# Kernel tuning notes

Measured on AMD Instinct MI355X. Metric: run time of the kernel, lower is better.

## Reference

```python
import jax, jax.numpy as jnp
import numpy as np

N_POINTS = 2097152
N_LEVELS = 16
F_PER_LEVEL = 2
LOG2_T = 19
T = 1 << LOG2_T            # 524288 entries per level
BASE_RES = 16
GROWTH = 1.5
PRIME_Y = np.uint32(2654435761)  # tcnn 2D spatial-hash prime (dim 0 prime is 1)


def _level_encode(x, tab, level):
    """Bilinear hash-grid lookup for one level. x: [N,2] in [0,1], tab: [T,F]."""
    scale = BASE_RES * GROWTH ** level - 1.0          # python float, static
    res = int(np.ceil(scale)) + 1                     # grid resolution (static)
    dense = res * res <= T                            # tcnn: dense if grid fits

    pos = x * jnp.asarray(scale, x.dtype) + 0.5       # [N,2]
    pg = jnp.floor(pos)
    frac = pos - pg                                   # [N,2] interpolation weights
    pg = pg.astype(jnp.uint32)

    out = jnp.zeros((x.shape[0], F_PER_LEVEL), x.dtype)
    for dx in (0, 1):
        for dy in (0, 1):
            cx = pg[:, 0] + np.uint32(dx)
            cy = pg[:, 1] + np.uint32(dy)
            if dense:
                idx = (cx + cy * np.uint32(res)) % np.uint32(T)
            else:
                idx = (cx ^ (cy * PRIME_Y)) % np.uint32(T)
            wx = frac[:, 0] if dx else 1.0 - frac[:, 0]
            wy = frac[:, 1] if dy else 1.0 - frac[:, 1]
            out = out + tab[idx.astype(jnp.int32)] * (wx * wy)[:, None]
    return out  # [N, F]


def setup_inputs() -> dict:
    key = jax.random.key(0)
    k1, k2 = jax.random.split(key)
    x = jax.random.uniform(k1, (N_POINTS, 2), dtype=jnp.float32)
    # tcnn initializes hash-grid params uniform in [-1e-4, 1e-4]
    table = jax.random.uniform(k2, (N_LEVELS, T, F_PER_LEVEL), dtype=jnp.float32,
                               minval=-1e-4, maxval=1e-4)
    return {"x": x, "table": table}


def reference(x, table):
    # multiresolution hash encoding: per-level bilinear gather, concat features
    outs = [_level_encode(x, table[l], l) for l in range(N_LEVELS)]
    return jnp.concatenate(outs, axis=-1)  # [N, N_LEVELS * F_PER_LEVEL] = [N, 32]
```

## Files before the change

### kernel.cpp

```cpp
#include <hip/hip_runtime.h>
#include <stdint.h>


constexpr int      kNPoints = 2097152;
constexpr uint32_t kT       = 524288u;
constexpr uint32_t kTMask   = kT - 1u;
constexpr uint32_t kPrimeY  = 2654435761u;

__device__ __host__ inline void level_consts(int l, float& sc, uint32_t& re, int& dense) {
    const float ksc[16] = {
        15.0f, 23.0f, 35.0f, 53.0f, 80.0f, 120.5f, 181.25f, 272.375f,
        409.0625f, 614.09375f, 921.640625f, 1382.9609375f,
        2074.94140625f, 3112.912109375f, 4669.8681640625f, 7005.30224609375f};
    const uint32_t kre[16] = {16u, 24u, 36u, 54u, 81u, 122u, 183u, 274u,
                              411u, 616u, 923u, 1384u, 2076u, 3114u, 4671u, 7007u};
    sc = ksc[l]; re = kre[l]; dense = (l < 10) ? 1 : 0;
}

__device__ __forceinline__ float2 encode_one(float2 xy, float scale, uint32_t res,
                                             int dense, const float2* __restrict__ tab) {
    const float px  = __fadd_rn(__fmul_rn(xy.x, scale), 0.5f);
    const float py  = __fadd_rn(__fmul_rn(xy.y, scale), 0.5f);
    const float fpx = floorf(px);
    const float fpy = floorf(py);
    const float fx  = px - fpx;
    const float fy  = py - fpy;
    const uint32_t gx = (uint32_t)fpx;
    const uint32_t gy = (uint32_t)fpy;

    float ax = 0.0f, ay = 0.0f;
#pragma unroll
    for (int dx = 0; dx < 2; ++dx) {
        const uint32_t cx = gx + (uint32_t)dx;
        const float    wx = dx ? fx : (1.0f - fx);
#pragma unroll
        for (int dy = 0; dy < 2; ++dy) {
            const uint32_t cy = gy + (uint32_t)dy;
            const float    wy = dy ? fy : (1.0f - fy);
            const uint32_t idx_d = (cx + cy * res) & kTMask;
            const uint32_t idx_h = (cx ^ (cy * kPrimeY)) & kTMask;
            const uint32_t idx   = dense ? idx_d : idx_h;
            const float2   v     = tab[idx];
            const float    w     = wx * wy;
            ax = fmaf(v.x, w, ax);
            ay = fmaf(v.y, w, ay);
        }
    }
    return make_float2(ax, ay);
}

__global__ __launch_bounds__(256) void level_kernel(
    const float* __restrict__ x,
    const float2* __restrict__ tab,
    float2* __restrict__ wsl,
    float scale, uint32_t res, int dense)
{
    const uint32_t n  = blockIdx.x * 256 + threadIdx.x;
    const float2   xy = reinterpret_cast<const float2*>(x)[n];
    const float2   r  = encode_one(xy, scale, res, dense, tab);
    union { float2 f2; unsigned long long u64; } p; p.f2 = r;
    __builtin_nontemporal_store(p.u64, reinterpret_cast<unsigned long long*>(wsl) + n);
}

template <int SPLIT>
__global__ __launch_bounds__(256) void merge_kernel(
    const float* __restrict__ x,
    const float* __restrict__ table,
    const float2* __restrict__ ws,
    float* __restrict__ out)
{
    __shared__ float s[256 * 36];
    const uint32_t tid = threadIdx.x;
    const uint32_t n   = blockIdx.x * 256 + tid;
    const float2   xy  = reinterpret_cast<const float2*>(x)[n];

#pragma unroll
    for (int l = 0; l < SPLIT; ++l) {
        float sc; uint32_t re; int de;
        level_consts(l, sc, re, de);
        const float2* tab = reinterpret_cast<const float2*>(table) + ((size_t)l << 19);
        const float2 r = encode_one(xy, sc, re, de, tab);
        s[tid * 36 + 2 * l]     = r.x;
        s[tid * 36 + 2 * l + 1] = r.y;
    }
#pragma unroll
    for (int j = 0; j < 16 - SPLIT; ++j) {
        const float2 v = ws[(size_t)j * kNPoints + n];
        s[tid * 36 + 2 * (SPLIT + j)]     = v.x;
        s[tid * 36 + 2 * (SPLIT + j) + 1] = v.y;
    }
    __syncthreads();

    float4* outb = reinterpret_cast<float4*>(out + (size_t)blockIdx.x * 8192);
#pragma unroll
    for (int k = 0; k < 8; ++k) {
        const uint32_t q   = tid + k * 256;
        const uint32_t row = q >> 3;
        const uint32_t c   = (q & 7u) * 4u;
        const float* sp = &s[row * 36 + c];
        outb[q] = make_float4(sp[0], sp[1], sp[2], sp[3]);
    }
}

__global__ __launch_bounds__(256) void hashgrid_fwd_fallback(
    const float* __restrict__ x,
    const float* __restrict__ table,
    float* __restrict__ out)
{
    const uint32_t tid = blockIdx.x * blockDim.x + threadIdx.x;
    const uint32_t l   = tid & 15u;
    const uint32_t n   = tid >> 4;
    float sc; uint32_t re; int de;
    level_consts((int)l, sc, re, de);
    const float2 xy = reinterpret_cast<const float2*>(x)[n];
    const float2* tab = reinterpret_cast<const float2*>(table) + ((size_t)l << 19);
    const float2 r = encode_one(xy, sc, re, de, tab);
    reinterpret_cast<float2*>(out)[tid] = r;
}

extern "C" void kernel_launch(void* const* d_in, const int* in_sizes, int n_in,
                              void* d_out, int out_size, void* d_ws, size_t ws_size,
                              hipStream_t stream) {
    const float* x     = (const float*)d_in[0];
    const float* table = (const float*)d_in[1];
    float*       out   = (float*)d_out;
    const int nblk = kNPoints / 256;

    const size_t need8 = (size_t)8 * kNPoints * sizeof(float2);
    const size_t need6 = (size_t)6 * kNPoints * sizeof(float2);

    if (ws_size >= need8) {
        float2* ws = (float2*)d_ws;
        for (int l = 8; l < 16; ++l) {
            float sc; uint32_t re; int de;
            level_consts(l, sc, re, de);
            level_kernel<<<nblk, 256, 0, stream>>>(
                x, reinterpret_cast<const float2*>(table) + ((size_t)l << 19),
                ws + (size_t)(l - 8) * kNPoints, sc, re, de);
        }
        merge_kernel<8><<<nblk, 256, 0, stream>>>(x, table, ws, out);
    } else if (ws_size >= need6) {
        float2* ws = (float2*)d_ws;
        for (int l = 10; l < 16; ++l) {
            float sc; uint32_t re; int de;
            level_consts(l, sc, re, de);
            level_kernel<<<nblk, 256, 0, stream>>>(
                x, reinterpret_cast<const float2*>(table) + ((size_t)l << 19),
                ws + (size_t)(l - 10) * kNPoints, sc, re, de);
        }
        merge_kernel<10><<<nblk, 256, 0, stream>>>(x, table, ws, out);
    } else {
        hashgrid_fwd_fallback<<<(kNPoints * 16) / 256, 256, 0, stream>>>(x, table, out);
    }
}
```

Measured before the change: 710.3 us.

## Fuse hashed-level launches into one interleaved kernel and halve merge LDS

Replaces eight per-level launches with a single kernel whose block index interleaves the eight hashed levels, so concurrently running blocks share L2 across levels and launch overhead is reduced. Each thread processes four points to raise memory-level parallelism. The merge kernel keeps all 16 results in registers and stages them through half-size shared memory in two passes, which should raise occupancy. Non-temporal loads and stores are used for the streaming x, workspace and output traffic. The trade-off is higher register pressure and an extra barrier, plus interleaving levels may thrash the cache, since all eight tables are accessed at once.

```diff
diff --git a/kernel.cpp b/kernel.cpp
--- a/kernel.cpp
+++ b/kernel.cpp
@@ -6,6 +6,24 @@
 constexpr uint32_t kT       = 524288u;
 constexpr uint32_t kTMask   = kT - 1u;
 constexpr uint32_t kPrimeY  = 2654435761u;
+
+typedef float vf4 __attribute__((ext_vector_type(4)));
+
+__device__ __forceinline__ float2 nt_load_f2(const float2* p) {
+    union { unsigned long long u; float2 f2; } u;
+    u.u = __builtin_nontemporal_load(reinterpret_cast<const unsigned long long*>(p));
+    return u.f2;
+}
+
+__device__ __forceinline__ void nt_store_f2(float2* p, float2 v) {
+    union { unsigned long long u; float2 f2; } u; u.f2 = v;
+    __builtin_nontemporal_store(u.u, reinterpret_cast<unsigned long long*>(p));
+}
+
+__device__ __forceinline__ void nt_store_f4(float* p, float a, float b, float c, float d) {
+    vf4 v; v.x = a; v.y = b; v.z = c; v.w = d;
+    __builtin_nontemporal_store(v, reinterpret_cast<vf4*>(p));
+}
 
 __device__ __host__ inline void level_consts(int l, float& sc, uint32_t& re, int& dense) {
     const float ksc[16] = {
@@ -49,56 +67,82 @@
     return make_float2(ax, ay);
 }
 
-__global__ __launch_bounds__(256) void level_kernel(
+__global__ __launch_bounds__(256) void hash8_kernel(
     const float* __restrict__ x,
-    const float2* __restrict__ tab,
-    float2* __restrict__ wsl,
-    float scale, uint32_t res, int dense)
+    const float* __restrict__ table,
+    float2* __restrict__ ws)
 {
-    const uint32_t n  = blockIdx.x * 256 + threadIdx.x;
-    const float2   xy = reinterpret_cast<const float2*>(x)[n];
-    const float2   r  = encode_one(xy, scale, res, dense, tab);
-    union { float2 f2; unsigned long long u64; } p; p.f2 = r;
-    __builtin_nontemporal_store(p.u64, reinterpret_cast<unsigned long long*>(wsl) + n);
+    const uint32_t slot  = blockIdx.x & 7u;
+    const uint32_t chunk = blockIdx.x >> 3;
+    const int      l     = 8 + (int)slot;
+    float sc; uint32_t re; int de;
+    level_consts(l, sc, re, de);
+    const float2* __restrict__ tab =
+        reinterpret_cast<const float2*>(table) + ((size_t)l << 19);
+    float2* __restrict__ wsl = ws + (size_t)slot * kNPoints;
+
+    const uint32_t base = chunk * 1024u + threadIdx.x;
+    const float2* __restrict__ xv = reinterpret_cast<const float2*>(x);
+
+    float2 xy[4];
+#pragma unroll
+    for (int k = 0; k < 4; ++k)
+        xy[k] = nt_load_f2(xv + base + (uint32_t)k * 256u);
+
+    float2 r[4];
+#pragma unroll
+    for (int k = 0; k < 4; ++k)
+        r[k] = encode_one(xy[k], sc, re, de, tab);
+
+#pragma unroll
+    for (int k = 0; k < 4; ++k)
+        nt_store_f2(wsl + base + (uint32_t)k * 256u, r[k]);
 }
 
-template <int SPLIT>
-__global__ __launch_bounds__(256) void merge_kernel(
+__global__ __launch_bounds__(256) void merge8_kernel(
     const float* __restrict__ x,
     const float* __restrict__ table,
     const float2* __restrict__ ws,
     float* __restrict__ out)
 {
-    __shared__ float s[256 * 36];
+    __shared__ float s[128 * 36];
     const uint32_t tid = threadIdx.x;
-    const uint32_t n   = blockIdx.x * 256 + tid;
-    const float2   xy  = reinterpret_cast<const float2*>(x)[n];
+    const uint32_t n   = blockIdx.x * 256u + tid;
+    const float2   xy  = nt_load_f2(reinterpret_cast<const float2*>(x) + n);
 
+    float2 r[16];
 #pragma unroll
-    for (int l = 0; l < SPLIT; ++l) {
+    for (int l = 0; l < 8; ++l) {
         float sc; uint32_t re; int de;
         level_consts(l, sc, re, de);
         const float2* tab = reinterpret_cast<const float2*>(table) + ((size_t)l << 19);
-        const float2 r = encode_one(xy, sc, re, de, tab);
-        s[tid * 36 + 2 * l]     = r.x;
-        s[tid * 36 + 2 * l + 1] = r.y;
+        r[l] = encode_one(xy, sc, re, de, tab);
     }
 #pragma unroll
-    for (int j = 0; j < 16 - SPLIT; ++j) {
-        const float2 v = ws[(size_t)j * kNPoints + n];
-        s[tid * 36 + 2 * (SPLIT + j)]     = v.x;
-        s[tid * 36 + 2 * (SPLIT + j) + 1] = v.y;
-    }
-    __syncthreads();
+    for (int j = 0; j < 8; ++j)
+        r[8 + j] = nt_load_f2(ws + (size_t)j * kNPoints + n);
 
-    float4* outb = reinterpret_cast<float4*>(out + (size_t)blockIdx.x * 8192);
 #pragma unroll
-    for (int k = 0; k < 8; ++k) {
-        const uint32_t q   = tid + k * 256;
-        const uint32_t row = q >> 3;
-        const uint32_t c   = (q & 7u) * 4u;
-        const float* sp = &s[row * 36 + c];
-        outb[q] = make_float4(sp[0], sp[1], sp[2], sp[3]);
+    for (int h = 0; h < 2; ++h) {
+        if ((tid >> 7) == (uint32_t)h) {
+            const uint32_t p = tid & 127u;
+#pragma unroll
+            for (int l = 0; l < 16; ++l) {
+                s[p * 36 + 2 * l]     = r[l].x;
+                s[p * 36 + 2 * l + 1] = r[l].y;
+            }
+        }
+        __syncthreads();
+        float* ob = out + (size_t)blockIdx.x * 8192 + (uint32_t)h * 4096u;
+#pragma unroll
+        for (int k = 0; k < 4; ++k) {
+            const uint32_t q   = tid + (uint32_t)k * 256u;
+            const uint32_t row = q >> 3;
+            const uint32_t c   = (q & 7u) * 4u;
+            const float* sp = &s[row * 36 + c];
+            nt_store_f4(ob + q * 4u, sp[0], sp[1], sp[2], sp[3]);
+        }
+        if (h == 0) __syncthreads();
     }
 }
 
@@ -124,31 +168,13 @@
     const float* x     = (const float*)d_in[0];
     const float* table = (const float*)d_in[1];
     float*       out   = (float*)d_out;
-    const int nblk = kNPoints / 256;
 
     const size_t need8 = (size_t)8 * kNPoints * sizeof(float2);
-    const size_t need6 = (size_t)6 * kNPoints * sizeof(float2);
 
     if (ws_size >= need8) {
         float2* ws = (float2*)d_ws;
-        for (int l = 8; l < 16; ++l) {
-            float sc; uint32_t re; int de;
-            level_consts(l, sc, re, de);
-            level_kernel<<<nblk, 256, 0, stream>>>(
-                x, reinterpret_cast<const float2*>(table) + ((size_t)l << 19),
-                ws + (size_t)(l - 8) * kNPoints, sc, re, de);
-        }
-        merge_kernel<8><<<nblk, 256, 0, stream>>>(x, table, ws, out);
-    } else if (ws_size >= need6) {
-        float2* ws = (float2*)d_ws;
-        for (int l = 10; l < 16; ++l) {
-            float sc; uint32_t re; int de;
-            level_consts(l, sc, re, de);
-            level_kernel<<<nblk, 256, 0, stream>>>(
-                x, reinterpret_cast<const float2*>(table) + ((size_t)l << 19),
-                ws + (size_t)(l - 10) * kNPoints, sc, re, de);
-        }
-        merge_kernel<10><<<nblk, 256, 0, stream>>>(x, table, ws, out);
+        hash8_kernel<<<16384, 256, 0, stream>>>(x, table, ws);
+        merge8_kernel<<<kNPoints / 256, 256, 0, stream>>>(x, table, ws, out);
     } else {
         hashgrid_fwd_fallback<<<(kNPoints * 16) / 256, 256, 0, stream>>>(x, table, out);
     }
```

Result: faster. 686.8 us (-3.3%).
